# Kernel tuning notes

Hardware: AMD Instinct MI355X
Metric: run time of the kernel (lower is better)

Reference implementation:

```python
import jax, jax.numpy as jnp
import numpy as np

D_MODEL = 1024
BATCH, SEQ = 4, 4096


def setup_inputs() -> dict:
    key = jax.random.key(0)
    ks = jax.random.split(key, 4)
    scale = 1.0 / np.sqrt(D_MODEL)  # lecun_normal-ish init for Dense kernels
    x = jax.random.normal(ks[0], (BATCH, SEQ, D_MODEL), dtype=jnp.float32)
    Wf = jax.random.normal(ks[1], (D_MODEL, D_MODEL), dtype=jnp.float32) * scale
    Wi = jax.random.normal(ks[2], (D_MODEL, D_MODEL), dtype=jnp.float32) * scale
    Wb = jax.random.normal(ks[3], (D_MODEL, D_MODEL), dtype=jnp.float32) * scale
    bf = jnp.full((D_MODEL,), -4.0, dtype=jnp.float32)  # forget bias -> f~0.018
    bi = jnp.full((D_MODEL,), 4.0, dtype=jnp.float32)   # input bias  -> i~0.982
    bb = jnp.zeros((D_MODEL,), dtype=jnp.float32)
    return {"x": x, "Wf": Wf, "bf": bf, "Wi": Wi, "bi": bi, "Wb": Wb, "bb": bb}


def _scan_combine(c1, c2):
    a1, b1 = c1
    a2, b2 = c2
    # linear recurrence composition: h = a2*(a1*h_prev + b1) + b2
    return a1 * a2, a2 * b1 + b2


def reference(x, Wf, bf, Wi, bi, Wb, bb):
    # gates + drive: [B, S, D]
    f = jax.nn.sigmoid(jnp.einsum('bsd,de->bse', x, Wf) + bf)
    i = jax.nn.sigmoid(jnp.einsum('bsd,de->bse', x, Wi) + bi)
    b = (jnp.einsum('bsd,de->bse', x, Wb) + bb) / jnp.sqrt(jnp.float32(x.shape[-1]))
    a = (1.0 - f).astype(jnp.complex64)
    b_gated = (i * b).astype(jnp.complex64)
    # parallel associative scan over time axis: h_t = a_t * h_{t-1} + b_t
    _, state = jax.lax.associative_scan(_scan_combine, (a, b_gated), axis=1)
    return state.real
```

## Files before the change

kernel.cpp:

```cpp
#include <hip/hip_runtime.h>
#include <cstdint>

#define D_MODEL 1024
#define BATCH 4
#define SEQ 4096
#define M_TOT (BATCH*SEQ)

#define BM 128
#define BN 128
#define BK 64
#define NKT (D_MODEL/BK)

#define XS_BYTES 16384
#define WG_BYTES 16384
#define TILE_BYTES (XS_BYTES + 3*WG_BYTES)
#define SMEM_BYTES (2*TILE_BYTES)

#define NCHUNK 64
#define CHUNK 64

typedef __bf16 bf16x8 __attribute__((ext_vector_type(8)));
typedef float f32x4 __attribute__((ext_vector_type(4)));
typedef unsigned short u16x8 __attribute__((ext_vector_type(8)));

static __device__ __forceinline__ unsigned short f2bf(float f) {
    unsigned int u = __float_as_uint(f);
    return (unsigned short)((u + 0x7fffu + ((u >> 16) & 1u)) >> 16);
}

__global__ void k_convert_x(const float* __restrict__ x, unsigned short* __restrict__ xb) {
    int i = blockIdx.x * 256 + threadIdx.x;
    const float4* p = (const float4*)x;
    float4 v0 = p[2*i], v1 = p[2*i+1];
    u16x8 r;
    r[0] = f2bf(v0.x); r[1] = f2bf(v0.y); r[2] = f2bf(v0.z); r[3] = f2bf(v0.w);
    r[4] = f2bf(v1.x); r[5] = f2bf(v1.y); r[6] = f2bf(v1.z); r[7] = f2bf(v1.w);
    *(u16x8*)(xb + (size_t)i * 8) = r;
}

__global__ void k_transpose_w(const float* __restrict__ Wf, const float* __restrict__ Wi,
                              const float* __restrict__ Wb, unsigned short* __restrict__ wt) {
    __shared__ float tile[32][33];
    int g = blockIdx.z;
    const float* W = (g == 0) ? Wf : (g == 1) ? Wi : Wb;
    int n0 = blockIdx.x * 32, k0 = blockIdx.y * 32;
    int tx = threadIdx.x, ty = threadIdx.y;
    for (int j = 0; j < 4; ++j)
        tile[ty + j*8][tx] = W[(size_t)(k0 + ty + j*8) * D_MODEL + n0 + tx];
    __syncthreads();
    for (int j = 0; j < 4; ++j) {
        int n = n0 + ty + j*8;
        wt[(size_t)g * D_MODEL * D_MODEL + (size_t)n * D_MODEL + k0 + tx] = f2bf(tile[tx][ty + j*8]);
    }
}

#define GL16(gp, lp) \
    __builtin_amdgcn_global_load_lds((const __attribute__((address_space(1))) void*)(gp), \
                                     (__attribute__((address_space(3))) void*)(lp), 16, 0, 0)

__launch_bounds__(512, 2)
__global__ void k_gemm_gates(const unsigned short* __restrict__ xb, const unsigned short* __restrict__ wt,
                             const float* __restrict__ bfv, const float* __restrict__ biv,
                             const float* __restrict__ bbv,
                             float* __restrict__ a_out, float* __restrict__ bg_out) {
    extern __shared__ char smem[];
    const int tid  = threadIdx.x;
    const int wave = tid >> 6;
    const int lane = tid & 63;
    const int lr = lane & 15, lg = lane >> 4;
    const int m0 = blockIdx.x * BM;
    const int n0 = blockIdx.y * BN;
    const int wrow = (wave >> 2) * 64;
    const int wcol = (wave & 3) * 32;

    const int srow = tid >> 3;
    const int scb  = ((tid & 7) * 16) ^ ((srow & 7) << 4);
    const unsigned short* s0 = xb + (size_t)(m0 + srow)      * D_MODEL + (scb >> 1);
    const unsigned short* s1 = xb + (size_t)(m0 + 64 + srow) * D_MODEL + (scb >> 1);
    const unsigned short* s2 = wt + 0ull*D_MODEL*D_MODEL + (size_t)(n0 + srow)      * D_MODEL + (scb >> 1);
    const unsigned short* s3 = wt + 0ull*D_MODEL*D_MODEL + (size_t)(n0 + 64 + srow) * D_MODEL + (scb >> 1);
    const unsigned short* s4 = wt + 1ull*D_MODEL*D_MODEL + (size_t)(n0 + srow)      * D_MODEL + (scb >> 1);
    const unsigned short* s5 = wt + 1ull*D_MODEL*D_MODEL + (size_t)(n0 + 64 + srow) * D_MODEL + (scb >> 1);
    const unsigned short* s6 = wt + 2ull*D_MODEL*D_MODEL + (size_t)(n0 + srow)      * D_MODEL + (scb >> 1);
    const unsigned short* s7 = wt + 2ull*D_MODEL*D_MODEL + (size_t)(n0 + 64 + srow) * D_MODEL + (scb >> 1);

#define STAGE(bufsel) do { \
        char* _b = smem + (bufsel)*TILE_BYTES + wave*1024; \
        GL16(s0, _b + 0*8192); GL16(s1, _b + 1*8192); \
        GL16(s2, _b + 2*8192); GL16(s3, _b + 3*8192); \
        GL16(s4, _b + 4*8192); GL16(s5, _b + 5*8192); \
        GL16(s6, _b + 6*8192); GL16(s7, _b + 7*8192); \
        s0 += BK; s1 += BK; s2 += BK; s3 += BK; \
        s4 += BK; s5 += BK; s6 += BK; s7 += BK; \
    } while (0)

    f32x4 acc[3][4][2] = {};
    const int sxor = (lr & 7) << 4;

    STAGE(0);
    __syncthreads();

    for (int kt = 0; kt < NKT; ++kt) {
        if (kt + 1 < NKT) STAGE((kt + 1) & 1);

        const char* tb = smem + (kt & 1) * TILE_BYTES;
        #pragma unroll
        for (int kk = 0; kk < 2; ++kk) {
            const int ko = (kk*64 + lg*16) ^ sxor;
            bf16x8 af[4];
            bf16x8 bw[3][2];
            #pragma unroll
            for (int mi = 0; mi < 4; ++mi)
                af[mi] = *(const bf16x8*)(tb + (wrow + mi*16 + lr)*128 + ko);
            #pragma unroll
            for (int g = 0; g < 3; ++g)
                #pragma unroll
                for (int ni = 0; ni < 2; ++ni)
                    bw[g][ni] = *(const bf16x8*)(tb + XS_BYTES + g*WG_BYTES +
                                                 (wcol + ni*16 + lr)*128 + ko);
            #pragma unroll
            for (int g = 0; g < 3; ++g)
                #pragma unroll
                for (int mi = 0; mi < 4; ++mi)
                    #pragma unroll
                    for (int ni = 0; ni < 2; ++ni)
                        acc[g][mi][ni] = __builtin_amdgcn_mfma_f32_16x16x32_bf16(
                            af[mi], bw[g][ni], acc[g][mi][ni], 0, 0, 0);
        }
        __syncthreads();
    }

    #pragma unroll
    for (int ni = 0; ni < 2; ++ni) {
        const int col = n0 + wcol + ni*16 + lr;
        const float vbf = bfv[col], vbi = biv[col], vbb = bbv[col];
        #pragma unroll
        for (int mi = 0; mi < 4; ++mi) {
            #pragma unroll
            for (int r = 0; r < 4; ++r) {
                const int row = m0 + wrow + mi*16 + lg*4 + r;
                const float zf = acc[0][mi][ni][r] + vbf;
                const float zi = acc[1][mi][ni][r] + vbi;
                const float zb = (acc[2][mi][ni][r] + vbb) * 0.03125f;
                const float a  = 1.0f / (1.0f + __expf(zf));
                const float ig = 1.0f / (1.0f + __expf(-zi));
                const size_t o = (size_t)row * D_MODEL + col;
                a_out[o]  = a;
                bg_out[o] = ig * zb;
            }
        }
    }
#undef STAGE
}

__global__ void k_chunk_local(const float* __restrict__ a, const float* __restrict__ bg,
                              float* __restrict__ Ac, float* __restrict__ Bc) {
    const int d = (blockIdx.x & 3) * 256 + threadIdx.x;
    const int c = (blockIdx.x >> 2) & 63;
    const int b = blockIdx.x >> 8;
    const size_t base = ((size_t)b * SEQ + (size_t)c * CHUNK) * D_MODEL + d;
    float A = 1.0f, Bv = 0.0f;
    for (int t = 0; t < CHUNK; ++t) {
        const float av = a[base + (size_t)t * D_MODEL];
        const float bv = bg[base + (size_t)t * D_MODEL];
        A *= av;
        Bv = fmaf(av, Bv, bv);
    }
    const size_t o = ((size_t)b * NCHUNK + c) * D_MODEL + d;
    Ac[o] = A;
    Bc[o] = Bv;
}

__global__ void k_chunk_prefix(const float* __restrict__ Ac, const float* __restrict__ Bc,
                               float* __restrict__ H) {
    const int d = (blockIdx.x & 3) * 256 + threadIdx.x;
    const int b = blockIdx.x >> 2;
    float h = 0.0f;
    for (int c = 0; c < NCHUNK; ++c) {
        const size_t o = ((size_t)b * NCHUNK + c) * D_MODEL + d;
        H[o] = h;
        h = fmaf(Ac[o], h, Bc[o]);
    }
}

__global__ void k_apply(const float* __restrict__ a, float* io, const float* __restrict__ H) {
    const int d = (blockIdx.x & 3) * 256 + threadIdx.x;
    const int c = (blockIdx.x >> 2) & 63;
    const int b = blockIdx.x >> 8;
    const size_t base = ((size_t)b * SEQ + (size_t)c * CHUNK) * D_MODEL + d;
    float h = H[((size_t)b * NCHUNK + c) * D_MODEL + d];
    for (int t = 0; t < CHUNK; ++t) {
        const size_t o = base + (size_t)t * D_MODEL;
        const float bv = io[o];
        h = fmaf(a[o], h, bv);
        io[o] = h;
    }
}

extern "C" void kernel_launch(void* const* d_in, const int* in_sizes, int n_in,
                              void* d_out, int out_size, void* d_ws, size_t ws_size,
                              hipStream_t stream) {
    const float* x   = (const float*)d_in[0];
    const float* Wf  = (const float*)d_in[1];
    const float* bfv = (const float*)d_in[2];
    const float* Wi  = (const float*)d_in[3];
    const float* biv = (const float*)d_in[4];
    const float* Wb  = (const float*)d_in[5];
    const float* bbv = (const float*)d_in[6];
    float* out = (float*)d_out;

    char* ws = (char*)d_ws;
    float*          a_buf = (float*)ws;
    unsigned short* xb    = (unsigned short*)(ws + (64ull << 20));
    unsigned short* wt    = (unsigned short*)(ws + (96ull << 20));
    float* Ac = (float*)(ws + (64ull << 20));
    float* Bc = (float*)(ws + (65ull << 20));
    float* Hb = (float*)(ws + (66ull << 20));
    float* bg_buf = out;

    static int smem_set = 0;
    if (!smem_set) {
        hipFuncSetAttribute((const void*)k_gemm_gates,
                            hipFuncAttributeMaxDynamicSharedMemorySize, SMEM_BYTES);
        smem_set = 1;
    }

    hipLaunchKernelGGL(k_convert_x, dim3((M_TOT * D_MODEL / 8) / 256), dim3(256), 0, stream, x, xb);
    hipLaunchKernelGGL(k_transpose_w, dim3(32, 32, 3), dim3(32, 8), 0, stream, Wf, Wi, Wb, wt);
    hipLaunchKernelGGL(k_gemm_gates, dim3(M_TOT / BM, D_MODEL / BN), dim3(512), SMEM_BYTES, stream,
                       xb, wt, bfv, biv, bbv, a_buf, bg_buf);
    hipLaunchKernelGGL(k_chunk_local, dim3(BATCH * NCHUNK * (D_MODEL / 256)), dim3(256), 0, stream,
                       a_buf, bg_buf, Ac, Bc);
    hipLaunchKernelGGL(k_chunk_prefix, dim3(BATCH * (D_MODEL / 256)), dim3(256), 0, stream,
                       Ac, Bc, Hb);
    hipLaunchKernelGGL(k_apply, dim3(BATCH * NCHUNK * (D_MODEL / 256)), dim3(256), 0, stream,
                       a_buf, bg_buf, Hb);
}
```

Baseline: 190.9 us.

## Use 4-wave single-buffered GEMM blocks with 64x64 per-wave tiles

The gate GEMM moves from 8 waves per block with double-buffered LDS to 4 waves per block, each computing a 64x64 tile for all three gates, with a single 64KB LDS buffer. The intent is to raise per-wave data reuse (fewer LDS reads per MFMA) and halve LDS use so more blocks fit per CU. The cost is lost overlap: each k-step now loads, synchronizes, computes, then synchronizes again, so global-load latency is exposed unless co-resident blocks hide it. The per-wave accumulator doubles to 192 floats, which increases register pressure.

```diff
diff --git a/kernel.cpp b/kernel.cpp
--- a/kernel.cpp
+++ b/kernel.cpp
@@ -13,8 +13,7 @@
 
 #define XS_BYTES 16384
 #define WG_BYTES 16384
-#define TILE_BYTES (XS_BYTES + 3*WG_BYTES)
-#define SMEM_BYTES (2*TILE_BYTES)
+#define SMEM_BYTES (XS_BYTES + 3*WG_BYTES)
 
 #define NCHUNK 64
 #define CHUNK 64
@@ -58,7 +57,7 @@
     __builtin_amdgcn_global_load_lds((const __attribute__((address_space(1))) void*)(gp), \
                                      (__attribute__((address_space(3))) void*)(lp), 16, 0, 0)
 
-__launch_bounds__(512, 2)
+__launch_bounds__(256, 2)
 __global__ void k_gemm_gates(const unsigned short* __restrict__ xb, const unsigned short* __restrict__ wt,
                              const float* __restrict__ bfv, const float* __restrict__ biv,
                              const float* __restrict__ bbv,
@@ -70,68 +69,72 @@
     const int lr = lane & 15, lg = lane >> 4;
     const int m0 = blockIdx.x * BM;
     const int n0 = blockIdx.y * BN;
-    const int wrow = (wave >> 2) * 64;
-    const int wcol = (wave & 3) * 32;
-
-    const int srow = tid >> 3;
-    const int scb  = ((tid & 7) * 16) ^ ((srow & 7) << 4);
-    const unsigned short* s0 = xb + (size_t)(m0 + srow)      * D_MODEL + (scb >> 1);
-    const unsigned short* s1 = xb + (size_t)(m0 + 64 + srow) * D_MODEL + (scb >> 1);
-    const unsigned short* s2 = wt + 0ull*D_MODEL*D_MODEL + (size_t)(n0 + srow)      * D_MODEL + (scb >> 1);
-    const unsigned short* s3 = wt + 0ull*D_MODEL*D_MODEL + (size_t)(n0 + 64 + srow) * D_MODEL + (scb >> 1);
-    const unsigned short* s4 = wt + 1ull*D_MODEL*D_MODEL + (size_t)(n0 + srow)      * D_MODEL + (scb >> 1);
-    const unsigned short* s5 = wt + 1ull*D_MODEL*D_MODEL + (size_t)(n0 + 64 + srow) * D_MODEL + (scb >> 1);
-    const unsigned short* s6 = wt + 2ull*D_MODEL*D_MODEL + (size_t)(n0 + srow)      * D_MODEL + (scb >> 1);
-    const unsigned short* s7 = wt + 2ull*D_MODEL*D_MODEL + (size_t)(n0 + 64 + srow) * D_MODEL + (scb >> 1);
-
-#define STAGE(bufsel) do { \
-        char* _b = smem + (bufsel)*TILE_BYTES + wave*1024; \
-        GL16(s0, _b + 0*8192); GL16(s1, _b + 1*8192); \
-        GL16(s2, _b + 2*8192); GL16(s3, _b + 3*8192); \
-        GL16(s4, _b + 4*8192); GL16(s5, _b + 5*8192); \
-        GL16(s6, _b + 6*8192); GL16(s7, _b + 7*8192); \
-        s0 += BK; s1 += BK; s2 += BK; s3 += BK; \
-        s4 += BK; s5 += BK; s6 += BK; s7 += BK; \
+    const int wrow = (wave >> 1) * 64;
+    const int wcol = (wave & 1) * 64;
+
+    const int srl = wave*8 + (lane >> 3);
+    const int scb = ((lane & 7) * 16) ^ ((srl & 7) << 4);
+    const size_t aoff = (size_t)(m0 + srl) * D_MODEL + (scb >> 1);
+    const size_t boff = (size_t)(n0 + srl) * D_MODEL + (scb >> 1);
+
+#define STAGE(kt) do { \
+        const int _ko = (kt) * BK; \
+        char* _d = smem + wave*1024; \
+        GL16(xb + aoff + 0*32*D_MODEL + _ko, _d + 0*4096); \
+        GL16(xb + aoff + 1*32*D_MODEL + _ko, _d + 1*4096); \
+        GL16(xb + aoff + 2*32*D_MODEL + _ko, _d + 2*4096); \
+        GL16(xb + aoff + 3*32*D_MODEL + _ko, _d + 3*4096); \
+        _Pragma("unroll") \
+        for (int g = 0; g < 3; ++g) { \
+            const unsigned short* _s = wt + (size_t)g*D_MODEL*D_MODEL + boff + _ko; \
+            char* _db = _d + XS_BYTES + g*WG_BYTES; \
+            GL16(_s + 0*32*D_MODEL, _db + 0*4096); \
+            GL16(_s + 1*32*D_MODEL, _db + 1*4096); \
+            GL16(_s + 2*32*D_MODEL, _db + 2*4096); \
+            GL16(_s + 3*32*D_MODEL, _db + 3*4096); \
+        } \
     } while (0)
 
-    f32x4 acc[3][4][2] = {};
+    f32x4 acc[3][4][4] = {};
     const int sxor = (lr & 7) << 4;
 
     STAGE(0);
     __syncthreads();
 
     for (int kt = 0; kt < NKT; ++kt) {
-        if (kt + 1 < NKT) STAGE((kt + 1) & 1);
-
-        const char* tb = smem + (kt & 1) * TILE_BYTES;
+        bf16x8 af[2][4];
         #pragma unroll
         for (int kk = 0; kk < 2; ++kk) {
             const int ko = (kk*64 + lg*16) ^ sxor;
-            bf16x8 af[4];
-            bf16x8 bw[3][2];
             #pragma unroll
             for (int mi = 0; mi < 4; ++mi)
-                af[mi] = *(const bf16x8*)(tb + (wrow + mi*16 + lr)*128 + ko);
+                af[kk][mi] = *(const bf16x8*)(smem + (wrow + mi*16 + lr)*128 + ko);
+        }
+        #pragma unroll
+        for (int g = 0; g < 3; ++g) {
             #pragma unroll
-            for (int g = 0; g < 3; ++g)
+            for (int ni = 0; ni < 4; ++ni) {
+                const char* brow = smem + XS_BYTES + g*WG_BYTES + (wcol + ni*16 + lr)*128;
+                bf16x8 b0 = *(const bf16x8*)(brow + ((0*64 + lg*16) ^ sxor));
+                bf16x8 b1 = *(const bf16x8*)(brow + ((1*64 + lg*16) ^ sxor));
                 #pragma unroll
-                for (int ni = 0; ni < 2; ++ni)
-                    bw[g][ni] = *(const bf16x8*)(tb + XS_BYTES + g*WG_BYTES +
-                                                 (wcol + ni*16 + lr)*128 + ko);
-            #pragma unroll
-            for (int g = 0; g < 3; ++g)
-                #pragma unroll
-                for (int mi = 0; mi < 4; ++mi)
-                    #pragma unroll
-                    for (int ni = 0; ni < 2; ++ni)
-                        acc[g][mi][ni] = __builtin_amdgcn_mfma_f32_16x16x32_bf16(
-                            af[mi], bw[g][ni], acc[g][mi][ni], 0, 0, 0);
+                for (int mi = 0; mi < 4; ++mi) {
+                    acc[g][mi][ni] = __builtin_amdgcn_mfma_f32_16x16x32_bf16(
+                        af[0][mi], b0, acc[g][mi][ni], 0, 0, 0);
+                    acc[g][mi][ni] = __builtin_amdgcn_mfma_f32_16x16x32_bf16(
+                        af[1][mi], b1, acc[g][mi][ni], 0, 0, 0);
+                }
+            }
         }
         __syncthreads();
+        if (kt + 1 < NKT) {
+            STAGE(kt + 1);
+            __syncthreads();
+        }
     }
 
     #pragma unroll
-    for (int ni = 0; ni < 2; ++ni) {
+    for (int ni = 0; ni < 4; ++ni) {
         const int col = n0 + wcol + ni*16 + lr;
         const float vbf = bfv[col], vbi = biv[col], vbb = bbv[col];
         #pragma unroll
@@ -218,16 +221,12 @@
     float* Hb = (float*)(ws + (66ull << 20));
     float* bg_buf = out;
 
-    static int smem_set = 0;
-    if (!smem_set) {
-        hipFuncSetAttribute((const void*)k_gemm_gates,
-                            hipFuncAttributeMaxDynamicSharedMemorySize, SMEM_BYTES);
-        smem_set = 1;
-    }
+    hipFuncSetAttribute((const void*)k_gemm_gates,
+                        hipFuncAttributeMaxDynamicSharedMemorySize, SMEM_BYTES);
 
     hipLaunchKernelGGL(k_convert_x, dim3((M_TOT * D_MODEL / 8) / 256), dim3(256), 0, stream, x, xb);
     hipLaunchKernelGGL(k_transpose_w, dim3(32, 32, 3), dim3(32, 8), 0, stream, Wf, Wi, Wb, wt);
-    hipLaunchKernelGGL(k_gemm_gates, dim3(M_TOT / BM, D_MODEL / BN), dim3(512), SMEM_BYTES, stream,
+    hipLaunchKernelGGL(k_gemm_gates, dim3(M_TOT / BM, D_MODEL / BN), dim3(256), SMEM_BYTES, stream,
                        xb, wt, bfv, biv, bbv, a_buf, bg_buf);
     hipLaunchKernelGGL(k_chunk_local, dim3(BATCH * NCHUNK * (D_MODEL / 256)), dim3(256), 0, stream,
                        a_buf, bg_buf, Ac, Bc);
```

Result: slower. 196.0 us (+2.7%).

## Fuse chunk-local scan into GEMM epilogue and double the M tile

Applied to the files above, without the earlier changes.

Raises the GEMM M tile to 256 rows so each workgroup covers whole 64-step chunks and reuses each staged weight tile across more rows. The per-chunk (A,B) scan summaries are now computed in the epilogue from register values, combined across lanes with shuffles, which removes the separate chunk_local kernel and its full re-read of the a and b_gated buffers. The larger tile doubles the accumulator registers and LDS use (160 KB double-buffered), so occupancy drops and spills are possible. The Ac/Bc/H workspace offsets move to avoid overlapping the bf16 x buffer.

```diff
diff --git a/kernel.cpp b/kernel.cpp
--- a/kernel.cpp
+++ b/kernel.cpp
@@ -6,13 +6,13 @@
 #define SEQ 4096
 #define M_TOT (BATCH*SEQ)
 
-#define BM 128
+#define BM 256
 #define BN 128
 #define BK 64
 #define NKT (D_MODEL/BK)
 
-#define XS_BYTES 16384
-#define WG_BYTES 16384
+#define XS_BYTES (BM*BK*2)
+#define WG_BYTES (BN*BK*2)
 #define TILE_BYTES (XS_BYTES + 3*WG_BYTES)
 #define SMEM_BYTES (2*TILE_BYTES)
 
@@ -62,7 +62,8 @@
 __global__ void k_gemm_gates(const unsigned short* __restrict__ xb, const unsigned short* __restrict__ wt,
                              const float* __restrict__ bfv, const float* __restrict__ biv,
                              const float* __restrict__ bbv,
-                             float* __restrict__ a_out, float* __restrict__ bg_out) {
+                             float* __restrict__ a_out, float* __restrict__ bg_out,
+                             float* __restrict__ Ac, float* __restrict__ Bc) {
     extern __shared__ char smem[];
     const int tid  = threadIdx.x;
     const int wave = tid >> 6;
@@ -70,48 +71,51 @@
     const int lr = lane & 15, lg = lane >> 4;
     const int m0 = blockIdx.x * BM;
     const int n0 = blockIdx.y * BN;
-    const int wrow = (wave >> 2) * 64;
-    const int wcol = (wave & 3) * 32;
+    const int wr = wave >> 2;
+    const int wc = wave & 3;
+    const int wrow = wr * 128;
+    const int wcol = wc * 32;
 
     const int srow = tid >> 3;
     const int scb  = ((tid & 7) * 16) ^ ((srow & 7) << 4);
-    const unsigned short* s0 = xb + (size_t)(m0 + srow)      * D_MODEL + (scb >> 1);
-    const unsigned short* s1 = xb + (size_t)(m0 + 64 + srow) * D_MODEL + (scb >> 1);
-    const unsigned short* s2 = wt + 0ull*D_MODEL*D_MODEL + (size_t)(n0 + srow)      * D_MODEL + (scb >> 1);
-    const unsigned short* s3 = wt + 0ull*D_MODEL*D_MODEL + (size_t)(n0 + 64 + srow) * D_MODEL + (scb >> 1);
-    const unsigned short* s4 = wt + 1ull*D_MODEL*D_MODEL + (size_t)(n0 + srow)      * D_MODEL + (scb >> 1);
-    const unsigned short* s5 = wt + 1ull*D_MODEL*D_MODEL + (size_t)(n0 + 64 + srow) * D_MODEL + (scb >> 1);
-    const unsigned short* s6 = wt + 2ull*D_MODEL*D_MODEL + (size_t)(n0 + srow)      * D_MODEL + (scb >> 1);
-    const unsigned short* s7 = wt + 2ull*D_MODEL*D_MODEL + (size_t)(n0 + 64 + srow) * D_MODEL + (scb >> 1);
-
-#define STAGE(bufsel) do { \
-        char* _b = smem + (bufsel)*TILE_BYTES + wave*1024; \
-        GL16(s0, _b + 0*8192); GL16(s1, _b + 1*8192); \
-        GL16(s2, _b + 2*8192); GL16(s3, _b + 3*8192); \
-        GL16(s4, _b + 4*8192); GL16(s5, _b + 5*8192); \
-        GL16(s6, _b + 6*8192); GL16(s7, _b + 7*8192); \
-        s0 += BK; s1 += BK; s2 += BK; s3 += BK; \
-        s4 += BK; s5 += BK; s6 += BK; s7 += BK; \
+    const size_t a0 = (size_t)(m0 +   0 + srow) * D_MODEL + (scb >> 1);
+    const size_t a1 = (size_t)(m0 +  64 + srow) * D_MODEL + (scb >> 1);
+    const size_t a2 = (size_t)(m0 + 128 + srow) * D_MODEL + (scb >> 1);
+    const size_t a3 = (size_t)(m0 + 192 + srow) * D_MODEL + (scb >> 1);
+    const size_t b0 = (size_t)(n0 +   0 + srow) * D_MODEL + (scb >> 1);
+    const size_t b1 = (size_t)(n0 +  64 + srow) * D_MODEL + (scb >> 1);
+    const unsigned short* w0 = wt;
+    const unsigned short* w1 = wt + 1ull*D_MODEL*D_MODEL;
+    const unsigned short* w2 = wt + 2ull*D_MODEL*D_MODEL;
+
+#define STAGE(bufsel, kt) do { \
+        const size_t _k = (size_t)(kt) * BK; \
+        char* _d = smem + (bufsel)*TILE_BYTES + wave*1024; \
+        GL16(xb + a0 + _k, _d + 0*8192); \
+        GL16(xb + a1 + _k, _d + 1*8192); \
+        GL16(xb + a2 + _k, _d + 2*8192); \
+        GL16(xb + a3 + _k, _d + 3*8192); \
+        GL16(w0 + b0 + _k, _d + 4*8192); \
+        GL16(w0 + b1 + _k, _d + 5*8192); \
+        GL16(w1 + b0 + _k, _d + 6*8192); \
+        GL16(w1 + b1 + _k, _d + 7*8192); \
+        GL16(w2 + b0 + _k, _d + 8*8192); \
+        GL16(w2 + b1 + _k, _d + 9*8192); \
     } while (0)
 
-    f32x4 acc[3][4][2] = {};
+    f32x4 acc[3][8][2] = {};
     const int sxor = (lr & 7) << 4;
 
-    STAGE(0);
+    STAGE(0, 0);
     __syncthreads();
 
     for (int kt = 0; kt < NKT; ++kt) {
-        if (kt + 1 < NKT) STAGE((kt + 1) & 1);
-
+        if (kt + 1 < NKT) STAGE((kt + 1) & 1, kt + 1);
         const char* tb = smem + (kt & 1) * TILE_BYTES;
         #pragma unroll
         for (int kk = 0; kk < 2; ++kk) {
             const int ko = (kk*64 + lg*16) ^ sxor;
-            bf16x8 af[4];
             bf16x8 bw[3][2];
-            #pragma unroll
-            for (int mi = 0; mi < 4; ++mi)
-                af[mi] = *(const bf16x8*)(tb + (wrow + mi*16 + lr)*128 + ko);
             #pragma unroll
             for (int g = 0; g < 3; ++g)
                 #pragma unroll
@@ -119,13 +123,15 @@
                     bw[g][ni] = *(const bf16x8*)(tb + XS_BYTES + g*WG_BYTES +
                                                  (wcol + ni*16 + lr)*128 + ko);
             #pragma unroll
-            for (int g = 0; g < 3; ++g)
+            for (int mi = 0; mi < 8; ++mi) {
+                bf16x8 afr = *(const bf16x8*)(tb + (wrow + mi*16 + lr)*128 + ko);
                 #pragma unroll
-                for (int mi = 0; mi < 4; ++mi)
+                for (int g = 0; g < 3; ++g)
                     #pragma unroll
                     for (int ni = 0; ni < 2; ++ni)
                         acc[g][mi][ni] = __builtin_amdgcn_mfma_f32_16x16x32_bf16(
-                            af[mi], bw[g][ni], acc[g][mi][ni], 0, 0, 0);
+                            afr, bw[g][ni], acc[g][mi][ni], 0, 0, 0);
+            }
         }
         __syncthreads();
     }
@@ -134,8 +140,10 @@
     for (int ni = 0; ni < 2; ++ni) {
         const int col = n0 + wcol + ni*16 + lr;
         const float vbf = bfv[col], vbi = biv[col], vbb = bbv[col];
+        float sA[2][4], sB[2][4];
         #pragma unroll
-        for (int mi = 0; mi < 4; ++mi) {
+        for (int mi = 0; mi < 8; ++mi) {
+            float Ap = 1.0f, Bp = 0.0f;
             #pragma unroll
             for (int r = 0; r < 4; ++r) {
                 const int row = m0 + wrow + mi*16 + lg*4 + r;
@@ -144,31 +152,39 @@
                 const float zb = (acc[2][mi][ni][r] + vbb) * 0.03125f;
                 const float a  = 1.0f / (1.0f + __expf(zf));
                 const float ig = 1.0f / (1.0f + __expf(-zi));
+                const float bg = ig * zb;
                 const size_t o = (size_t)row * D_MODEL + col;
                 a_out[o]  = a;
-                bg_out[o] = ig * zb;
-            }
+                bg_out[o] = bg;
+                Bp = fmaf(a, Bp, bg);
+                Ap *= a;
+            }
+            sA[mi >> 2][mi & 3] = Ap;
+            sB[mi >> 2][mi & 3] = Bp;
         }
+        #pragma unroll
+        for (int half = 0; half < 2; ++half) {
+            float CA = 1.0f, CB = 0.0f;
+            #pragma unroll
+            for (int q = 0; q < 4; ++q) {
+                float A = sA[half][q], B = sB[half][q];
+                float Ao = __shfl_xor(A, 16), Bo = __shfl_xor(B, 16);
+                float B1 = (lg & 1) ? fmaf(A, Bo, B) : fmaf(Ao, B, Bo);
+                float A1 = A * Ao;
+                Ao = __shfl_xor(A1, 32); Bo = __shfl_xor(B1, 32);
+                float B2 = (lg & 2) ? fmaf(A1, Bo, B1) : fmaf(Ao, B1, Bo);
+                float A2 = A1 * Ao;
+                CB = fmaf(A2, CB, B2);
+                CA = CA * A2;
+            }
+            if (lg == 0) {
+                const int chG = blockIdx.x * 4 + wr * 2 + half;
+                Ac[(size_t)chG * D_MODEL + col] = CA;
+                Bc[(size_t)chG * D_MODEL + col] = CB;
+            }
+        }
     }
 #undef STAGE
-}
-
-__global__ void k_chunk_local(const float* __restrict__ a, const float* __restrict__ bg,
-                              float* __restrict__ Ac, float* __restrict__ Bc) {
-    const int d = (blockIdx.x & 3) * 256 + threadIdx.x;
-    const int c = (blockIdx.x >> 2) & 63;
-    const int b = blockIdx.x >> 8;
-    const size_t base = ((size_t)b * SEQ + (size_t)c * CHUNK) * D_MODEL + d;
-    float A = 1.0f, Bv = 0.0f;
-    for (int t = 0; t < CHUNK; ++t) {
-        const float av = a[base + (size_t)t * D_MODEL];
-        const float bv = bg[base + (size_t)t * D_MODEL];
-        A *= av;
-        Bv = fmaf(av, Bv, bv);
-    }
-    const size_t o = ((size_t)b * NCHUNK + c) * D_MODEL + d;
-    Ac[o] = A;
-    Bc[o] = Bv;
 }
 
 __global__ void k_chunk_prefix(const float* __restrict__ Ac, const float* __restrict__ Bc,
@@ -213,24 +229,18 @@
     float*          a_buf = (float*)ws;
     unsigned short* xb    = (unsigned short*)(ws + (64ull << 20));
     unsigned short* wt    = (unsigned short*)(ws + (96ull << 20));
-    float* Ac = (float*)(ws + (64ull << 20));
-    float* Bc = (float*)(ws + (65ull << 20));
-    float* Hb = (float*)(ws + (66ull << 20));
+    float* Ac = (float*)(ws + (102ull << 20));
+    float* Bc = (float*)(ws + (103ull << 20));
+    float* Hb = (float*)(ws + (64ull << 20));
     float* bg_buf = out;
 
-    static int smem_set = 0;
-    if (!smem_set) {
-        hipFuncSetAttribute((const void*)k_gemm_gates,
-                            hipFuncAttributeMaxDynamicSharedMemorySize, SMEM_BYTES);
-        smem_set = 1;
-    }
+    hipFuncSetAttribute((const void*)k_gemm_gates,
+                        hipFuncAttributeMaxDynamicSharedMemorySize, SMEM_BYTES);
 
     hipLaunchKernelGGL(k_convert_x, dim3((M_TOT * D_MODEL / 8) / 256), dim3(256), 0, stream, x, xb);
     hipLaunchKernelGGL(k_transpose_w, dim3(32, 32, 3), dim3(32, 8), 0, stream, Wf, Wi, Wb, wt);
     hipLaunchKernelGGL(k_gemm_gates, dim3(M_TOT / BM, D_MODEL / BN), dim3(512), SMEM_BYTES, stream,
-                       xb, wt, bfv, biv, bbv, a_buf, bg_buf);
-    hipLaunchKernelGGL(k_chunk_local, dim3(BATCH * NCHUNK * (D_MODEL / 256)), dim3(256), 0, stream,
-                       a_buf, bg_buf, Ac, Bc);
+                       xb, wt, bfv, biv, bbv, a_buf, bg_buf, Ac, Bc);
     hipLaunchKernelGGL(k_chunk_prefix, dim3(BATCH * (D_MODEL / 256)), dim3(256), 0, stream,
                        Ac, Bc, Hb);
     hipLaunchKernelGGL(k_apply, dim3(BATCH * NCHUNK * (D_MODEL / 256)), dim3(256), 0, stream,
```

After: 202.9 us. 1.06x slower.

## Fuse chunk-local scan into GEMM epilogue and store gates as bf16

Applied to the files above, without the earlier changes.

The GEMM epilogue now computes the per-chunk (A, B) scan summaries with warp shuffles across each 64-row wave tile, which removes the separate chunk_local kernel and its full re-read of the gate tensors. The intermediate forget gate and gated drive are stored as bf16 rather than fp32, halving intermediate traffic, and the apply kernel reads them packed and writes the fp32 output directly. The A-fragment loads in the MFMA loop are also split into two halves to lower register pressure. The epilogue grows longer, and the bf16 intermediates lower precision (the chunk summaries are computed from the rounded values so they stay consistent).

```diff
diff --git a/kernel.cpp b/kernel.cpp
--- a/kernel.cpp
+++ b/kernel.cpp
@@ -26,6 +26,9 @@
 static __device__ __forceinline__ unsigned short f2bf(float f) {
     unsigned int u = __float_as_uint(f);
     return (unsigned short)((u + 0x7fffu + ((u >> 16) & 1u)) >> 16);
+}
+static __device__ __forceinline__ float ubf(unsigned short u) {
+    return __uint_as_float((unsigned int)u << 16);
 }
 
 __global__ void k_convert_x(const float* __restrict__ x, unsigned short* __restrict__ xb) {
@@ -62,7 +65,8 @@
 __global__ void k_gemm_gates(const unsigned short* __restrict__ xb, const unsigned short* __restrict__ wt,
                              const float* __restrict__ bfv, const float* __restrict__ biv,
                              const float* __restrict__ bbv,
-                             float* __restrict__ a_out, float* __restrict__ bg_out) {
+                             unsigned short* __restrict__ f_out, unsigned short* __restrict__ bg_out,
+                             float* __restrict__ Ac, float* __restrict__ Bc) {
     extern __shared__ char smem[];
     const int tid  = threadIdx.x;
     const int wave = tid >> 6;
@@ -70,7 +74,8 @@
     const int lr = lane & 15, lg = lane >> 4;
     const int m0 = blockIdx.x * BM;
     const int n0 = blockIdx.y * BN;
-    const int wrow = (wave >> 2) * 64;
+    const int wr = wave >> 2;
+    const int wrow = wr * 64;
     const int wcol = (wave & 3) * 32;
 
     const int srow = tid >> 3;
@@ -107,10 +112,10 @@
         #pragma unroll
         for (int kk = 0; kk < 2; ++kk) {
             const int ko = (kk*64 + lg*16) ^ sxor;
-            bf16x8 af[4];
+            bf16x8 af[2];
             bf16x8 bw[3][2];
             #pragma unroll
-            for (int mi = 0; mi < 4; ++mi)
+            for (int mi = 0; mi < 2; ++mi)
                 af[mi] = *(const bf16x8*)(tb + (wrow + mi*16 + lr)*128 + ko);
             #pragma unroll
             for (int g = 0; g < 3; ++g)
@@ -121,11 +126,23 @@
             #pragma unroll
             for (int g = 0; g < 3; ++g)
                 #pragma unroll
-                for (int mi = 0; mi < 4; ++mi)
+                for (int mi = 0; mi < 2; ++mi)
                     #pragma unroll
                     for (int ni = 0; ni < 2; ++ni)
                         acc[g][mi][ni] = __builtin_amdgcn_mfma_f32_16x16x32_bf16(
                             af[mi], bw[g][ni], acc[g][mi][ni], 0, 0, 0);
+            bf16x8 af2[2];
+            #pragma unroll
+            for (int mi = 0; mi < 2; ++mi)
+                af2[mi] = *(const bf16x8*)(tb + (wrow + (mi+2)*16 + lr)*128 + ko);
+            #pragma unroll
+            for (int g = 0; g < 3; ++g)
+                #pragma unroll
+                for (int mi = 0; mi < 2; ++mi)
+                    #pragma unroll
+                    for (int ni = 0; ni < 2; ++ni)
+                        acc[g][mi+2][ni] = __builtin_amdgcn_mfma_f32_16x16x32_bf16(
+                            af2[mi], bw[g][ni], acc[g][mi+2][ni], 0, 0, 0);
         }
         __syncthreads();
     }
@@ -134,41 +151,50 @@
     for (int ni = 0; ni < 2; ++ni) {
         const int col = n0 + wcol + ni*16 + lr;
         const float vbf = bfv[col], vbi = biv[col], vbb = bbv[col];
+        float qA[4], qB[4];
         #pragma unroll
         for (int mi = 0; mi < 4; ++mi) {
+            float Ap = 1.0f, Bp = 0.0f;
             #pragma unroll
             for (int r = 0; r < 4; ++r) {
                 const int row = m0 + wrow + mi*16 + lg*4 + r;
                 const float zf = acc[0][mi][ni][r] + vbf;
                 const float zi = acc[1][mi][ni][r] + vbi;
                 const float zb = (acc[2][mi][ni][r] + vbb) * 0.03125f;
-                const float a  = 1.0f / (1.0f + __expf(zf));
+                const float fg = 1.0f / (1.0f + __expf(-zf));
                 const float ig = 1.0f / (1.0f + __expf(-zi));
+                const unsigned short fu  = f2bf(fg);
+                const unsigned short bgu = f2bf(ig * zb);
+                const float a_r  = 1.0f - ubf(fu);
+                const float bg_r = ubf(bgu);
                 const size_t o = (size_t)row * D_MODEL + col;
-                a_out[o]  = a;
-                bg_out[o] = ig * zb;
+                f_out[o]  = fu;
+                bg_out[o] = bgu;
+                Bp = fmaf(a_r, Bp, bg_r);
+                Ap *= a_r;
             }
+            qA[mi] = Ap; qB[mi] = Bp;
+        }
+        float CA = 1.0f, CB = 0.0f;
+        #pragma unroll
+        for (int q = 0; q < 4; ++q) {
+            float A = qA[q], B = qB[q];
+            float Ao = __shfl_xor(A, 16), Bo = __shfl_xor(B, 16);
+            float B1 = (lg & 1) ? fmaf(A, Bo, B) : fmaf(Ao, B, Bo);
+            float A1 = A * Ao;
+            Ao = __shfl_xor(A1, 32); Bo = __shfl_xor(B1, 32);
+            float B2 = (lg & 2) ? fmaf(A1, Bo, B1) : fmaf(Ao, B1, Bo);
+            float A2 = A1 * Ao;
+            CB = fmaf(A2, CB, B2);
+            CA = CA * A2;
+        }
+        if (lg == 0) {
+            const int chG = blockIdx.x * 2 + wr;
+            Ac[(size_t)chG * D_MODEL + col] = CA;
+            Bc[(size_t)chG * D_MODEL + col] = CB;
         }
     }
 #undef STAGE
-}
-
-__global__ void k_chunk_local(const float* __restrict__ a, const float* __restrict__ bg,
-                              float* __restrict__ Ac, float* __restrict__ Bc) {
-    const int d = (blockIdx.x & 3) * 256 + threadIdx.x;
-    const int c = (blockIdx.x >> 2) & 63;
-    const int b = blockIdx.x >> 8;
-    const size_t base = ((size_t)b * SEQ + (size_t)c * CHUNK) * D_MODEL + d;
-    float A = 1.0f, Bv = 0.0f;
-    for (int t = 0; t < CHUNK; ++t) {
-        const float av = a[base + (size_t)t * D_MODEL];
-        const float bv = bg[base + (size_t)t * D_MODEL];
-        A *= av;
-        Bv = fmaf(av, Bv, bv);
-    }
-    const size_t o = ((size_t)b * NCHUNK + c) * D_MODEL + d;
-    Ac[o] = A;
-    Bc[o] = Bv;
 }
 
 __global__ void k_chunk_prefix(const float* __restrict__ Ac, const float* __restrict__ Bc,
@@ -183,17 +209,25 @@
     }
 }
 
-__global__ void k_apply(const float* __restrict__ a, float* io, const float* __restrict__ H) {
-    const int d = (blockIdx.x & 3) * 256 + threadIdx.x;
-    const int c = (blockIdx.x >> 2) & 63;
-    const int b = blockIdx.x >> 8;
-    const size_t base = ((size_t)b * SEQ + (size_t)c * CHUNK) * D_MODEL + d;
-    float h = H[((size_t)b * NCHUNK + c) * D_MODEL + d];
+__global__ void k_apply(const unsigned short* __restrict__ f, const unsigned short* __restrict__ bg,
+                        const float* __restrict__ H, float* __restrict__ out) {
+    const int d0 = (blockIdx.x & 1) * 512 + threadIdx.x * 2;
+    const int c = (blockIdx.x >> 1) & 63;
+    const int b = blockIdx.x >> 7;
+    const size_t base = ((size_t)b * SEQ + (size_t)c * CHUNK) * D_MODEL + d0;
+    const size_t hoff = ((size_t)b * NCHUNK + c) * D_MODEL + d0;
+    float h0 = H[hoff], h1 = H[hoff + 1];
     for (int t = 0; t < CHUNK; ++t) {
         const size_t o = base + (size_t)t * D_MODEL;
-        const float bv = io[o];
-        h = fmaf(a[o], h, bv);
-        io[o] = h;
+        const unsigned int fv = *(const unsigned int*)(f + o);
+        const unsigned int gv = *(const unsigned int*)(bg + o);
+        const float a0 = 1.0f - __uint_as_float(fv << 16);
+        const float a1 = 1.0f - __uint_as_float(fv & 0xffff0000u);
+        const float b0 = __uint_as_float(gv << 16);
+        const float b1 = __uint_as_float(gv & 0xffff0000u);
+        h0 = fmaf(a0, h0, b0);
+        h1 = fmaf(a1, h1, b1);
+        *(float2*)(out + o) = make_float2(h0, h1);
     }
 }
 
@@ -210,29 +244,23 @@
     float* out = (float*)d_out;
 
     char* ws = (char*)d_ws;
-    float*          a_buf = (float*)ws;
+    unsigned short* fbuf  = (unsigned short*)ws;
+    unsigned short* bgbuf = (unsigned short*)(ws + (32ull << 20));
     unsigned short* xb    = (unsigned short*)(ws + (64ull << 20));
     unsigned short* wt    = (unsigned short*)(ws + (96ull << 20));
-    float* Ac = (float*)(ws + (64ull << 20));
-    float* Bc = (float*)(ws + (65ull << 20));
-    float* Hb = (float*)(ws + (66ull << 20));
-    float* bg_buf = out;
-
-    static int smem_set = 0;
-    if (!smem_set) {
-        hipFuncSetAttribute((const void*)k_gemm_gates,
-                            hipFuncAttributeMaxDynamicSharedMemorySize, SMEM_BYTES);
-        smem_set = 1;
-    }
+    float* Ac = (float*)(ws + (102ull << 20));
+    float* Bc = (float*)(ws + (103ull << 20));
+    float* Hb = (float*)(ws + (64ull << 20));
+
+    hipFuncSetAttribute((const void*)k_gemm_gates,
+                        hipFuncAttributeMaxDynamicSharedMemorySize, SMEM_BYTES);
 
     hipLaunchKernelGGL(k_convert_x, dim3((M_TOT * D_MODEL / 8) / 256), dim3(256), 0, stream, x, xb);
     hipLaunchKernelGGL(k_transpose_w, dim3(32, 32, 3), dim3(32, 8), 0, stream, Wf, Wi, Wb, wt);
     hipLaunchKernelGGL(k_gemm_gates, dim3(M_TOT / BM, D_MODEL / BN), dim3(512), SMEM_BYTES, stream,
-                       xb, wt, bfv, biv, bbv, a_buf, bg_buf);
-    hipLaunchKernelGGL(k_chunk_local, dim3(BATCH * NCHUNK * (D_MODEL / 256)), dim3(256), 0, stream,
-                       a_buf, bg_buf, Ac, Bc);
+                       xb, wt, bfv, biv, bbv, fbuf, bgbuf, Ac, Bc);
     hipLaunchKernelGGL(k_chunk_prefix, dim3(BATCH * (D_MODEL / 256)), dim3(256), 0, stream,
                        Ac, Bc, Hb);
-    hipLaunchKernelGGL(k_apply, dim3(BATCH * NCHUNK * (D_MODEL / 256)), dim3(256), 0, stream,
-                       a_buf, bg_buf, Hb);
-}
+    hipLaunchKernelGGL(k_apply, dim3(BATCH * NCHUNK * 2), dim3(256), 0, stream,
+                       fbuf, bgbuf, Hb, out);
+}
```

Result: faster. 163.7 us (-14.3%).
